# Optimization experiments

Measured on AMD Instinct MI355X. Metric: run time of the kernel, lower is better.

## Reference

```python
import jax, jax.numpy as jnp
import numpy as np

DIM = 1024
N_HEADS = 16
HEAD_DIM = DIM // N_HEADS  # 64
THETA = 10000.0
B, S = 4, 1024


def _rope_full_dim(x):
    """RoPE applied over the FULL last dim (head_dim == model dim), matching the
    original module which builds RotaryEmbeddings(head_dim=args.dim) and applies
    it to [B, S, dim] before splitting into heads. Positions start at 0."""
    Bx, Sx, D = x.shape
    freq = 1.0 / (THETA ** (jnp.arange(0, D, 2, dtype=jnp.float32) / D))  # [D/2]
    ang = jnp.arange(Sx, dtype=jnp.float32)[:, None] * freq[None, :]      # [S, D/2]
    cos, sin = jnp.cos(ang), jnp.sin(ang)
    xp = x.astype(jnp.float32).reshape(Bx, Sx, D // 2, 2)
    x0, x1 = xp[..., 0], xp[..., 1]
    rot = jnp.stack([x0 * cos - x1 * sin, x0 * sin + x1 * cos], axis=-1)
    return rot.reshape(Bx, Sx, D).astype(x.dtype)


def setup_inputs() -> dict:
    key = jax.random.key(0)
    ks = jax.random.split(key, 5)
    scale = 1.0 / np.sqrt(DIM)
    x = jax.random.normal(ks[0], (B, S, DIM), dtype=jnp.float32)
    Wq = jax.random.normal(ks[1], (DIM, DIM), dtype=jnp.float32) * scale
    Wk = jax.random.normal(ks[2], (DIM, DIM), dtype=jnp.float32) * scale
    Wv = jax.random.normal(ks[3], (DIM, DIM), dtype=jnp.float32) * scale
    Wo = jax.random.normal(ks[4], (DIM, DIM), dtype=jnp.float32) * scale
    bo = jnp.zeros((DIM,), dtype=jnp.float32)
    return {"x": x, "Wq": Wq, "Wk": Wk, "Wv": Wv, "Wo": Wo, "bo": bo, "start_pos": 0}


def reference(x, Wq, Wk, Wv, Wo, bo, start_pos):
    # start_pos == 0: the zero-initialized KV cache write+read is an identity
    # (keys == xk, values == xv over [:, :S]); n_rep == 1 so repeat_kv is a no-op.
    # NOTE: the original applies NO causal mask.
    Bx, Sx, _ = x.shape
    xq = _rope_full_dim(x @ Wq.T)  # [B, S, DIM] (weights stored torch-style [out,in])
    xk = _rope_full_dim(x @ Wk.T)
    xv = x @ Wv.T
    q = xq.reshape(Bx, Sx, N_HEADS, HEAD_DIM).transpose(0, 2, 1, 3)  # [B,H,S,D]
    k = xk.reshape(Bx, Sx, N_HEADS, HEAD_DIM).transpose(0, 2, 1, 3)
    v = xv.reshape(Bx, Sx, N_HEADS, HEAD_DIM).transpose(0, 2, 1, 3)
    scores = jnp.einsum("bhqd,bhkd->bhqk", q, k) / np.float32(np.sqrt(HEAD_DIM))
    attn = jax.nn.softmax(scores.astype(jnp.float32), axis=-1).astype(q.dtype)
    out = jnp.einsum("bhqk,bhkd->bhqd", attn, v)          # [B,H,S,D]
    out = out.transpose(0, 2, 1, 3).reshape(Bx, Sx, DIM)  # [B,S,DIM]
    return out @ Wo.T + bo
```

## Files before the change

### kernel.cpp

```cpp
#include <hip/hip_runtime.h>
#include <cstdint>
#include <cstddef>

typedef _Float16 f16;
typedef __attribute__((ext_vector_type(8))) _Float16 h8v;
typedef __attribute__((ext_vector_type(4))) _Float16 h4v;
typedef __attribute__((ext_vector_type(2))) _Float16 h2v;
typedef __attribute__((ext_vector_type(4))) float f4v;

#define DIM 1024
#define SEQ 1024
#define NH 16
#define HD 64

#if __has_builtin(__builtin_amdgcn_exp2f)
#define EXP2(x) __builtin_amdgcn_exp2f(x)
#else
#define EXP2(x) exp2f(x)
#endif
#if __has_builtin(__builtin_amdgcn_rcpf)
#define RCP(x) __builtin_amdgcn_rcpf(x)
#else
#define RCP(x) (1.0f / (x))
#endif

__device__ __forceinline__ void gld16(const void* g, void* l) {
  __builtin_amdgcn_global_load_lds(
      (const __attribute__((address_space(1))) void*)g,
      (__attribute__((address_space(3))) void*)l, 16, 0, 0);
}

__device__ __forceinline__ f4v mfma16(h8v a, h8v b, f4v c) {
  return __builtin_amdgcn_mfma_f32_16x16x32_f16(a, b, c, 0, 0, 0);
}
__device__ __forceinline__ f4v mfma16k16(h4v a, h4v b, f4v c) {
  return __builtin_amdgcn_mfma_f32_16x16x16f16(a, b, c, 0, 0, 0);
}

__device__ __forceinline__ h4v pk4(float a, float b, float c, float d) {
  h2v lo = __builtin_bit_cast(h2v, __builtin_amdgcn_cvt_pkrtz(a, b));
  h2v hi = __builtin_bit_cast(h2v, __builtin_amdgcn_cvt_pkrtz(c, d));
  return (h4v){lo[0], lo[1], hi[0], hi[1]};
}

__device__ __forceinline__ void cvt_store4(f16* dst, float4 v) {
  *(h4v*)dst = (h4v){(f16)v.x, (f16)v.y, (f16)v.z, (f16)v.w};
}

__global__ __launch_bounds__(256) void convert_kernel(
    const float* __restrict__ x,  const float* __restrict__ Wq,
    const float* __restrict__ Wk, const float* __restrict__ Wv,
    const float* __restrict__ Wo,
    f16* __restrict__ xh, f16* __restrict__ wqkv, f16* __restrict__ woh)
{
  int i = blockIdx.x * 256 + threadIdx.x;
  cvt_store4(xh + 4 * (size_t)i, ((const float4*)x)[i]);
  if (i < DIM * DIM / 4) {
    cvt_store4(wqkv + 4 * (size_t)i,               ((const float4*)Wq)[i]);
    cvt_store4(wqkv + DIM * DIM + 4 * (size_t)i,   ((const float4*)Wk)[i]);
    cvt_store4(wqkv + 2 * DIM * DIM + 4 * (size_t)i, ((const float4*)Wv)[i]);
    cvt_store4(woh + 4 * (size_t)i,                ((const float4*)Wo)[i]);
  }
}

__global__ __launch_bounds__(256) void qkv_gemm(
    const f16* __restrict__ A, const f16* __restrict__ W,
    f16* __restrict__ Qh, f16* __restrict__ Kh, f16* __restrict__ Vt)
{
  __shared__ f16 lA[2][4096];
  __shared__ f16 lB[2][4096];
  const int m0 = blockIdx.x * 128;
  const int n0 = blockIdx.y * 128;
  const int tid = threadIdx.x;
  const int w = tid >> 6, lane = tid & 63, quad = lane >> 4, l16 = lane & 15;
  const int wm = (w >> 1) * 64, wn = (w & 1) * 64;

  const int c0 = tid, c1 = 256 + tid;
  const int r0 = c0 >> 2, kc0 = (c0 & 3) ^ ((r0 >> 1) & 3);
  const int r1 = c1 >> 2, kc1 = (c1 & 3) ^ ((r1 >> 1) & 3);
  const f16* gA0 = A + (size_t)(m0 + r0) * DIM + kc0 * 8;
  const f16* gA1 = A + (size_t)(m0 + r1) * DIM + kc1 * 8;
  const f16* gB0 = W + (size_t)(n0 + r0) * DIM + kc0 * 8;
  const f16* gB1 = W + (size_t)(n0 + r1) * DIM + kc1 * 8;
  const int d0 = (c0 & ~63) * 8, d1 = (c1 & ~63) * 8;

  int pA[4], pB[4];
#pragma unroll
  for (int t = 0; t < 4; ++t) {
    int r = wm + t * 16 + l16;
    pA[t] = r * 4 + (quad ^ ((r >> 1) & 3));
    int rn = wn + t * 16 + l16;
    pB[t] = rn * 4 + (quad ^ ((rn >> 1) & 3));
  }

  f4v acc[4][4] = {};

#define QKV_PREF(KT, BUF)                  \
  {                                        \
    const int ko = (KT) * 32;              \
    gld16(gA0 + ko, &lA[BUF][d0]);         \
    gld16(gA1 + ko, &lA[BUF][d1]);         \
    gld16(gB0 + ko, &lB[BUF][d0]);         \
    gld16(gB1 + ko, &lB[BUF][d1]);         \
  }

#define QKV_COMP(BUF)                                                \
  {                                                                  \
    h8v af[4], bf[4];                                                \
    _Pragma("unroll")                                                \
    for (int t = 0; t < 4; ++t) af[t] = *(const h8v*)&lA[BUF][pA[t] * 8]; \
    _Pragma("unroll")                                                \
    for (int t = 0; t < 4; ++t) bf[t] = *(const h8v*)&lB[BUF][pB[t] * 8]; \
    _Pragma("unroll")                                                \
    for (int i = 0; i < 4; ++i)                                      \
      _Pragma("unroll")                                              \
      for (int j = 0; j < 4; ++j)                                    \
        acc[i][j] = mfma16(af[i], bf[j], acc[i][j]);                 \
  }

  QKV_PREF(0, 0);
  for (int kt = 0; kt < DIM / 32; kt += 2) {
    __syncthreads();
    QKV_PREF(kt + 1, 1);
    QKV_COMP(0);
    __syncthreads();
    if (kt + 2 < DIM / 32) QKV_PREF(kt + 2, 0);
    QKV_COMP(1);
  }
#undef QKV_PREF
#undef QKV_COMP

  if (n0 < 2 * DIM) {
    f16* dst = (n0 < DIM) ? Qh : Kh;
    const float osc = (n0 < DIM) ? 0.18033688f : 1.0f;
#pragma unroll
    for (int i = 0; i < 4; ++i) {
      const int mb = m0 + wm + i * 16 + quad * 4;
#pragma unroll
      for (int j = 0; j < 4; ++j) {
        const int n = n0 + wn + j * 16 + l16;
        const int d = n & (DIM - 1);
        const float fr = exp2f(-0.025952563f * (float)(d >> 1));
        const float sgn = (d & 1) ? 1.0f : -1.0f;
        const int hh = d >> 6, dd = d & 63;
#pragma unroll
        for (int r = 0; r < 4; ++r) {
          const int m = mb + r;
          const int s = m & (SEQ - 1), b = m >> 10;
          const float v = acc[i][j][r];
          const float pt = __shfl_xor(v, 1, 64);
          float sn, cs;
          __sincosf((float)s * fr, &sn, &cs);
          dst[((size_t)(b * NH + hh) * SEQ + s) * HD + dd] =
              (f16)((v * cs + sgn * pt * sn) * osc);
        }
      }
    }
  } else {
#pragma unroll
    for (int i = 0; i < 4; ++i) {
      const int mb = m0 + wm + i * 16 + quad * 4;
      const int b = mb >> 10;
      const int sp = ((mb & (SEQ - 1)) & ~63) + quad * 16 + i * 4;
#pragma unroll
      for (int j = 0; j < 4; ++j) {
        const int d = (n0 - 2 * DIM) + wn + j * 16 + l16;
        const int hh = d >> 6, dd = d & 63;
        h4v vv = {(f16)acc[i][j][0], (f16)acc[i][j][1],
                  (f16)acc[i][j][2], (f16)acc[i][j][3]};
        *(h4v*)&Vt[((size_t)(b * NH + hh) * HD + dd) * SEQ + sp] = vv;
      }
    }
  }
}

__global__ __launch_bounds__(512) void attn_kernel(
    const f16* __restrict__ Q, const f16* __restrict__ K,
    const f16* __restrict__ V, f16* __restrict__ O)
{
  __shared__ f16 LK[2][4096];
  __shared__ f16 LV[2][4096];
  const int tid = threadIdx.x;
  const int w = tid >> 6, lane = tid & 63, quad = lane >> 4, l16 = lane & 15;
  const int bid = blockIdx.x;
  const int qt = bid >> 6, bh = bid & 63;
  const f16* Qb = Q + (size_t)bh * SEQ * HD;
  const f16* Kg = K + (size_t)bh * SEQ * HD;
  const f16* Vg = V + (size_t)bh * HD * SEQ;
  const int q0 = qt * 128 + w * 16;

  const h8v bq0a = *(const h8v*)&Qb[(size_t)(q0 + l16) * HD + quad * 8];
  const h8v bq0b = *(const h8v*)&Qb[(size_t)(q0 + l16) * HD + quad * 8 + 32];

  const int c0 = tid;
  const int r0 = c0 >> 3, kc0 = (c0 & 7) ^ (r0 & 7);
  const f16* gK0 = Kg + (size_t)r0 * HD + kc0 * 8;
  const f16* gV0 = Vg + (size_t)r0 * SEQ + kc0 * 8;
  const int dk0 = (c0 & ~63) * 8;

  int koff[4][2];
#pragma unroll
  for (int j = 0; j < 4; ++j) {
    int r = j * 16 + l16;
#pragma unroll
    for (int kk = 0; kk < 2; ++kk)
      koff[j][kk] = (r * 8 + ((quad + 4 * kk) ^ (r & 7))) * 8;
  }
  int voff2[2];
#pragma unroll
  for (int jp = 0; jp < 2; ++jp)
    voff2[jp] = l16 * 64 + ((quad * 2 + jp) ^ (l16 & 7)) * 8;

  const h4v vones = {(f16)1.f, (f16)1.f, (f16)1.f, (f16)1.f};
  f4v accL0 = {};
  f4v accO0[4] = {};

#define ATTN_PREF(TT, BUF)                       \
  {                                              \
    const size_t kb = (size_t)(TT) * 64;         \
    gld16(gK0 + kb * HD, &LK[BUF][dk0]);         \
    gld16(gV0 + kb, &LV[BUF][dk0]);              \
  }

#define ATTN_TILE(BUF)                                                       \
  {                                                                          \
    h8v kf[4][2];                                                            \
    _Pragma("unroll")                                                        \
    for (int j = 0; j < 4; ++j) {                                            \
      kf[j][0] = *(const h8v*)&LK[BUF][koff[j][0]];                          \
      kf[j][1] = *(const h8v*)&LK[BUF][koff[j][1]];                          \
    }                                                                        \
    f4v sc0[4];                                                              \
    _Pragma("unroll")                                                        \
    for (int j = 0; j < 4; ++j) {                                            \
      f4v z0 = {-12.f, -12.f, -12.f, -12.f};          \
      z0 = mfma16(kf[j][0], bq0a, z0);                                       \
      z0 = mfma16(kf[j][1], bq0b, z0);                                       \
      sc0[j] = z0;                                                           \
    }                                                                        \
    h4v pf0[4];                                                              \
    _Pragma("unroll")                                                        \
    for (int j = 0; j < 4; ++j) {                                            \
      pf0[j] = pk4(EXP2(sc0[j][0]), EXP2(sc0[j][1]),                         \
                   EXP2(sc0[j][2]), EXP2(sc0[j][3]));                        \
    }                                                                        \
    h4v ps0 = (pf0[0] + pf0[1]) + (pf0[2] + pf0[3]);                         \
    accL0 = mfma16k16(ps0, vones, accL0);                                    \
    _Pragma("unroll")                                                        \
    for (int dt = 0; dt < 4; ++dt) {                                         \
      _Pragma("unroll")                                                      \
      for (int jp = 0; jp < 2; ++jp) {                                       \
        const h8v vv = *(const h8v*)&LV[BUF][voff2[jp] + dt * 1024];         \
        const h4v vlo = __builtin_shufflevector(vv, vv, 0, 1, 2, 3);         \
        const h4v vhi = __builtin_shufflevector(vv, vv, 4, 5, 6, 7);         \
        accO0[dt] = mfma16k16(pf0[2 * jp], vlo, accO0[dt]);                  \
        accO0[dt] = mfma16k16(pf0[2 * jp + 1], vhi, accO0[dt]);              \
      }                                                                      \
    }                                                                        \
  }

  ATTN_PREF(0, 0);
  for (int t = 0; t < SEQ / 64; t += 2) {
    __syncthreads();
    ATTN_PREF(t + 1, 1);
    ATTN_TILE(0);
    __syncthreads();
    if (t + 2 < SEQ / 64) ATTN_PREF(t + 2, 0);
    ATTN_TILE(1);
  }
#undef ATTN_PREF
#undef ATTN_TILE

  f4v inv0;
#pragma unroll
  for (int r = 0; r < 4; ++r) inv0[r] = RCP(accL0[r]);

  const int b = bh >> 4, hh = bh & 15;
#pragma unroll
  for (int dt = 0; dt < 4; ++dt) {
    const int d = dt * 16 + l16;
#pragma unroll
    for (int r = 0; r < 4; ++r) {
      const int s0 = q0 + quad * 4 + r;
      O[(size_t)(b * SEQ + s0) * DIM + hh * HD + d] =
          (f16)(accO0[dt][r] * inv0[r]);
    }
  }
}

__global__ __launch_bounds__(256) void out_gemm(
    const f16* __restrict__ A, const f16* __restrict__ W,
    const float* __restrict__ bias, float* __restrict__ out)
{
  __shared__ f16 lA[2][2048];
  __shared__ f16 lB[2][4096];
  const int m0 = blockIdx.x * 64;
  const int n0 = blockIdx.y * 128;
  const int tid = threadIdx.x;
  const int w = tid >> 6, lane = tid & 63, quad = lane >> 4, l16 = lane & 15;
  const int wm = (w >> 1) * 32, wn = (w & 1) * 64;

  const int c0 = tid, c1 = 256 + tid;
  const int rA = c0 >> 2, kcA = (c0 & 3) ^ ((rA >> 1) & 3);
  const int rB1 = c1 >> 2, kcB1 = (c1 & 3) ^ ((rB1 >> 1) & 3);
  const f16* gA  = A + (size_t)(m0 + rA) * DIM + kcA * 8;
  const f16* gB0 = W + (size_t)(n0 + rA) * DIM + kcA * 8;
  const f16* gB1 = W + (size_t)(n0 + rB1) * DIM + kcB1 * 8;
  const int dA = (c0 & ~63) * 8, dB1 = (c1 & ~63) * 8;

  int pA_[2], pB_[4];
#pragma unroll
  for (int t = 0; t < 2; ++t) {
    int r = wm + t * 16 + l16;
    pA_[t] = r * 4 + (quad ^ ((r >> 1) & 3));
  }
#pragma unroll
  for (int t = 0; t < 4; ++t) {
    int rn = wn + t * 16 + l16;
    pB_[t] = rn * 4 + (quad ^ ((rn >> 1) & 3));
  }

  f4v acc[2][4] = {};

#define OUT_PREF(KT, BUF)                  \
  {                                        \
    const int ko = (KT) * 32;              \
    gld16(gA + ko, &lA[BUF][dA]);          \
    gld16(gB0 + ko, &lB[BUF][dA]);         \
    gld16(gB1 + ko, &lB[BUF][dB1]);        \
  }

#define OUT_COMP(BUF)                                                 \
  {                                                                   \
    h8v af[2], bf[4];                                                 \
    _Pragma("unroll")                                                 \
    for (int t = 0; t < 2; ++t) af[t] = *(const h8v*)&lA[BUF][pA_[t] * 8]; \
    _Pragma("unroll")                                                 \
    for (int t = 0; t < 4; ++t) bf[t] = *(const h8v*)&lB[BUF][pB_[t] * 8]; \
    _Pragma("unroll")                                                 \
    for (int i = 0; i < 2; ++i)                                       \
      _Pragma("unroll")                                               \
      for (int j = 0; j < 4; ++j)                                     \
        acc[i][j] = mfma16(af[i], bf[j], acc[i][j]);                  \
  }

  OUT_PREF(0, 0);
  for (int kt = 0; kt < DIM / 32; kt += 2) {
    __syncthreads();
    OUT_PREF(kt + 1, 1);
    OUT_COMP(0);
    __syncthreads();
    if (kt + 2 < DIM / 32) OUT_PREF(kt + 2, 0);
    OUT_COMP(1);
  }
#undef OUT_PREF
#undef OUT_COMP

#pragma unroll
  for (int i = 0; i < 2; ++i) {
#pragma unroll
    for (int j = 0; j < 4; ++j) {
      const int n = n0 + wn + j * 16 + l16;
      const float bv = bias[n];
#pragma unroll
      for (int r = 0; r < 4; ++r) {
        const int m = m0 + wm + i * 16 + quad * 4 + r;
        out[(size_t)m * DIM + n] = acc[i][j][r] + bv;
      }
    }
  }
}

extern "C" void kernel_launch(void* const* d_in, const int* in_sizes, int n_in,
                              void* d_out, int out_size, void* d_ws, size_t ws_size,
                              hipStream_t stream)
{
  (void)in_sizes; (void)n_in; (void)out_size; (void)ws_size;
  const float* x  = (const float*)d_in[0];
  const float* Wq = (const float*)d_in[1];
  const float* Wk = (const float*)d_in[2];
  const float* Wv = (const float*)d_in[3];
  const float* Wo = (const float*)d_in[4];
  const float* bo = (const float*)d_in[5];
  float* out = (float*)d_out;

  char* ws = (char*)d_ws;
  const size_t MB = (size_t)1 << 20;
  f16* xh   = (f16*)(ws);
  f16* wqkv = (f16*)(ws + 8  * MB);
  f16* woh  = (f16*)(ws + 14 * MB);
  f16* Qh   = (f16*)(ws + 16 * MB);
  f16* Kh   = (f16*)(ws + 24 * MB);
  f16* Vt   = (f16*)(ws + 32 * MB);
  f16* Oh   = (f16*)(ws);

  convert_kernel<<<dim3(4096), 256, 0, stream>>>(x, Wq, Wk, Wv, Wo, xh, wqkv, woh);
  qkv_gemm<<<dim3(32, 24), 256, 0, stream>>>(xh, wqkv, Qh, Kh, Vt);
  attn_kernel<<<dim3(512), 512, 0, stream>>>(Qh, Kh, Vt, Oh);
  out_gemm<<<dim3(64, 8), 256, 0, stream>>>(Oh, woh, bo, out);
}
```

Baseline: 172.6 us.

## Fuse fp32-to-fp16 conversion into GEMM tile loads, drop convert kernel

Removes the separate conversion kernel and has the QKV and output GEMMs stream fp32 inputs and weights directly into shared memory, converting to fp16 when fragments are read for MFMA. This saves one launch and a full write and reread of the fp16 copies. In exchange each GEMM moves twice the bytes per tile from global memory, uses twice the LDS, which may lower occupancy, and repeats conversion work on every tile reuse.

```diff
diff --git a/kernel.cpp b/kernel.cpp
--- a/kernel.cpp
+++ b/kernel.cpp
@@ -43,74 +43,73 @@
   return (h4v){lo[0], lo[1], hi[0], hi[1]};
 }
 
-__device__ __forceinline__ void cvt_store4(f16* dst, float4 v) {
-  *(h4v*)dst = (h4v){(f16)v.x, (f16)v.y, (f16)v.z, (f16)v.w};
-}
-
-__global__ __launch_bounds__(256) void convert_kernel(
+__device__ __forceinline__ h8v cvt8(f4v a, f4v b) {
+  return (h8v){(f16)a[0], (f16)a[1], (f16)a[2], (f16)a[3],
+               (f16)b[0], (f16)b[1], (f16)b[2], (f16)b[3]};
+}
+
+__global__ __launch_bounds__(256) void qkv_gemm(
     const float* __restrict__ x,  const float* __restrict__ Wq,
     const float* __restrict__ Wk, const float* __restrict__ Wv,
-    const float* __restrict__ Wo,
-    f16* __restrict__ xh, f16* __restrict__ wqkv, f16* __restrict__ woh)
-{
-  int i = blockIdx.x * 256 + threadIdx.x;
-  cvt_store4(xh + 4 * (size_t)i, ((const float4*)x)[i]);
-  if (i < DIM * DIM / 4) {
-    cvt_store4(wqkv + 4 * (size_t)i,               ((const float4*)Wq)[i]);
-    cvt_store4(wqkv + DIM * DIM + 4 * (size_t)i,   ((const float4*)Wk)[i]);
-    cvt_store4(wqkv + 2 * DIM * DIM + 4 * (size_t)i, ((const float4*)Wv)[i]);
-    cvt_store4(woh + 4 * (size_t)i,                ((const float4*)Wo)[i]);
-  }
-}
-
-__global__ __launch_bounds__(256) void qkv_gemm(
-    const f16* __restrict__ A, const f16* __restrict__ W,
     f16* __restrict__ Qh, f16* __restrict__ Kh, f16* __restrict__ Vt)
 {
-  __shared__ f16 lA[2][4096];
-  __shared__ f16 lB[2][4096];
+  __shared__ __align__(16) float lAf[2][4096];
+  __shared__ __align__(16) float lBf[2][4096];
   const int m0 = blockIdx.x * 128;
   const int n0 = blockIdx.y * 128;
   const int tid = threadIdx.x;
   const int w = tid >> 6, lane = tid & 63, quad = lane >> 4, l16 = lane & 15;
   const int wm = (w >> 1) * 64, wn = (w & 1) * 64;
 
-  const int c0 = tid, c1 = 256 + tid;
-  const int r0 = c0 >> 2, kc0 = (c0 & 3) ^ ((r0 >> 1) & 3);
-  const int r1 = c1 >> 2, kc1 = (c1 & 3) ^ ((r1 >> 1) & 3);
-  const f16* gA0 = A + (size_t)(m0 + r0) * DIM + kc0 * 8;
-  const f16* gA1 = A + (size_t)(m0 + r1) * DIM + kc1 * 8;
-  const f16* gB0 = W + (size_t)(n0 + r0) * DIM + kc0 * 8;
-  const f16* gB1 = W + (size_t)(n0 + r1) * DIM + kc1 * 8;
-  const int d0 = (c0 & ~63) * 8, d1 = (c1 & ~63) * 8;
+  const float* Wsel = (n0 < DIM) ? Wq : (n0 < 2 * DIM) ? Wk : Wv;
+  const int nr = n0 & (DIM - 1);
+
+  const float* gAf[4];
+  const float* gBf[4];
+  int dls[4];
+#pragma unroll
+  for (int i = 0; i < 4; ++i) {
+    const int c = tid + 256 * i;
+    const int r = c >> 3;
+    const int col = ((c & 7) ^ (((c >> 4) & 3) << 1)) * 4;
+    gAf[i] = x + (size_t)(m0 + r) * DIM + col;
+    gBf[i] = Wsel + (size_t)(nr + r) * DIM + col;
+    dls[i] = (c & ~63) * 4;
+  }
 
   int pA[4], pB[4];
 #pragma unroll
   for (int t = 0; t < 4; ++t) {
     int r = wm + t * 16 + l16;
-    pA[t] = r * 4 + (quad ^ ((r >> 1) & 3));
+    pA[t] = r * 32 + (quad ^ ((r >> 1) & 3)) * 8;
     int rn = wn + t * 16 + l16;
-    pB[t] = rn * 4 + (quad ^ ((rn >> 1) & 3));
+    pB[t] = rn * 32 + (quad ^ ((rn >> 1) & 3)) * 8;
   }
 
   f4v acc[4][4] = {};
 
-#define QKV_PREF(KT, BUF)                  \
-  {                                        \
-    const int ko = (KT) * 32;              \
-    gld16(gA0 + ko, &lA[BUF][d0]);         \
-    gld16(gA1 + ko, &lA[BUF][d1]);         \
-    gld16(gB0 + ko, &lB[BUF][d0]);         \
-    gld16(gB1 + ko, &lB[BUF][d1]);         \
+#define QKV_PREF(KT, BUF)                          \
+  {                                                \
+    const int ko = (KT) * 32;                      \
+    _Pragma("unroll")                              \
+    for (int i = 0; i < 4; ++i) {                  \
+      gld16(gAf[i] + ko, &lAf[BUF][dls[i]]);       \
+      gld16(gBf[i] + ko, &lBf[BUF][dls[i]]);       \
+    }                                              \
   }
 
 #define QKV_COMP(BUF)                                                \
   {                                                                  \
     h8v af[4], bf[4];                                                \
     _Pragma("unroll")                                                \
-    for (int t = 0; t < 4; ++t) af[t] = *(const h8v*)&lA[BUF][pA[t] * 8]; \
-    _Pragma("unroll")                                                \
-    for (int t = 0; t < 4; ++t) bf[t] = *(const h8v*)&lB[BUF][pB[t] * 8]; \
+    for (int t = 0; t < 4; ++t) {                                    \
+      f4v lo = *(const f4v*)&lAf[BUF][pA[t]];                        \
+      f4v hi = *(const f4v*)&lAf[BUF][pA[t] + 4];                    \
+      af[t] = cvt8(lo, hi);                                          \
+      f4v lo2 = *(const f4v*)&lBf[BUF][pB[t]];                       \
+      f4v hi2 = *(const f4v*)&lBf[BUF][pB[t] + 4];                   \
+      bf[t] = cvt8(lo2, hi2);                                        \
+    }                                                                \
     _Pragma("unroll")                                                \
     for (int i = 0; i < 4; ++i)                                      \
       _Pragma("unroll")                                              \
@@ -289,24 +288,32 @@
 }
 
 __global__ __launch_bounds__(256) void out_gemm(
-    const f16* __restrict__ A, const f16* __restrict__ W,
+    const f16* __restrict__ A, const float* __restrict__ W,
     const float* __restrict__ bias, float* __restrict__ out)
 {
   __shared__ f16 lA[2][2048];
-  __shared__ f16 lB[2][4096];
+  __shared__ __align__(16) float lBf[2][4096];
   const int m0 = blockIdx.x * 64;
   const int n0 = blockIdx.y * 128;
   const int tid = threadIdx.x;
   const int w = tid >> 6, lane = tid & 63, quad = lane >> 4, l16 = lane & 15;
   const int wm = (w >> 1) * 32, wn = (w & 1) * 64;
 
-  const int c0 = tid, c1 = 256 + tid;
+  const int c0 = tid;
   const int rA = c0 >> 2, kcA = (c0 & 3) ^ ((rA >> 1) & 3);
-  const int rB1 = c1 >> 2, kcB1 = (c1 & 3) ^ ((rB1 >> 1) & 3);
-  const f16* gA  = A + (size_t)(m0 + rA) * DIM + kcA * 8;
-  const f16* gB0 = W + (size_t)(n0 + rA) * DIM + kcA * 8;
-  const f16* gB1 = W + (size_t)(n0 + rB1) * DIM + kcB1 * 8;
-  const int dA = (c0 & ~63) * 8, dB1 = (c1 & ~63) * 8;
+  const f16* gA = A + (size_t)(m0 + rA) * DIM + kcA * 8;
+  const int dA = (c0 & ~63) * 8;
+
+  const float* gBf[4];
+  int dlsB[4];
+#pragma unroll
+  for (int i = 0; i < 4; ++i) {
+    const int c = tid + 256 * i;
+    const int r = c >> 3;
+    const int col = ((c & 7) ^ (((c >> 4) & 3) << 1)) * 4;
+    gBf[i] = W + (size_t)(n0 + r) * DIM + col;
+    dlsB[i] = (c & ~63) * 4;
+  }
 
   int pA_[2], pB_[4];
 #pragma unroll
@@ -317,17 +324,18 @@
 #pragma unroll
   for (int t = 0; t < 4; ++t) {
     int rn = wn + t * 16 + l16;
-    pB_[t] = rn * 4 + (quad ^ ((rn >> 1) & 3));
+    pB_[t] = rn * 32 + (quad ^ ((rn >> 1) & 3)) * 8;
   }
 
   f4v acc[2][4] = {};
 
-#define OUT_PREF(KT, BUF)                  \
-  {                                        \
-    const int ko = (KT) * 32;              \
-    gld16(gA + ko, &lA[BUF][dA]);          \
-    gld16(gB0 + ko, &lB[BUF][dA]);         \
-    gld16(gB1 + ko, &lB[BUF][dB1]);        \
+#define OUT_PREF(KT, BUF)                            \
+  {                                                  \
+    const int ko = (KT) * 32;                        \
+    gld16(gA + ko, &lA[BUF][dA]);                    \
+    _Pragma("unroll")                                \
+    for (int i = 0; i < 4; ++i)                      \
+      gld16(gBf[i] + ko, &lBf[BUF][dlsB[i]]);        \
   }
 
 #define OUT_COMP(BUF)                                                 \
@@ -336,7 +344,11 @@
     _Pragma("unroll")                                                 \
     for (int t = 0; t < 2; ++t) af[t] = *(const h8v*)&lA[BUF][pA_[t] * 8]; \
     _Pragma("unroll")                                                 \
-    for (int t = 0; t < 4; ++t) bf[t] = *(const h8v*)&lB[BUF][pB_[t] * 8]; \
+    for (int t = 0; t < 4; ++t) {                                     \
+      f4v lo = *(const f4v*)&lBf[BUF][pB_[t]];                        \
+      f4v hi = *(const f4v*)&lBf[BUF][pB_[t] + 4];                    \
+      bf[t] = cvt8(lo, hi);                                           \
+    }                                                                 \
     _Pragma("unroll")                                                 \
     for (int i = 0; i < 2; ++i)                                       \
       _Pragma("unroll")                                               \
@@ -386,16 +398,12 @@
 
   char* ws = (char*)d_ws;
   const size_t MB = (size_t)1 << 20;
-  f16* xh   = (f16*)(ws);
-  f16* wqkv = (f16*)(ws + 8  * MB);
-  f16* woh  = (f16*)(ws + 14 * MB);
-  f16* Qh   = (f16*)(ws + 16 * MB);
-  f16* Kh   = (f16*)(ws + 24 * MB);
-  f16* Vt   = (f16*)(ws + 32 * MB);
-  f16* Oh   = (f16*)(ws);
-
-  convert_kernel<<<dim3(4096), 256, 0, stream>>>(x, Wq, Wk, Wv, Wo, xh, wqkv, woh);
-  qkv_gemm<<<dim3(32, 24), 256, 0, stream>>>(xh, wqkv, Qh, Kh, Vt);
+  f16* Qh = (f16*)(ws);
+  f16* Kh = (f16*)(ws + 8 * MB);
+  f16* Vt = (f16*)(ws + 16 * MB);
+  f16* Oh = (f16*)(ws + 24 * MB);
+
+  qkv_gemm<<<dim3(32, 24), 256, 0, stream>>>(x, Wq, Wk, Wv, Qh, Kh, Vt);
   attn_kernel<<<dim3(512), 512, 0, stream>>>(Qh, Kh, Vt, Oh);
-  out_gemm<<<dim3(64, 8), 256, 0, stream>>>(Oh, woh, bo, out);
-}
+  out_gemm<<<dim3(64, 8), 256, 0, stream>>>(Oh, Wo, bo, out);
+}
```

Measured after the change: 189.6 us. 9.9% more time.
